# Kernel tuning notes

Measured on AMD Instinct MI355X. Metric: run time of the kernel, lower is better.

Reference implementation:

```python
import jax, jax.numpy as jnp
import numpy as np

B, S, I, C, N, V, O = 32, 256, 256, 512, 1024, 64, 256
EPS = 1e-12


def setup_inputs() -> dict:
    key = jax.random.key(0)
    ks = iter(jax.random.split(key, 40))

    def rn(shape, scale=0.05):
        return (jax.random.normal(next(ks), shape, jnp.float32) * scale)

    inp = {
        'x': jax.random.normal(next(ks), (B, S, I), jnp.float32),
        # LSTM controller (PyTorch gate order i,f,g,o)
        'lstm_Wih': rn((4 * C, I + V)), 'lstm_Whh': rn((4 * C, C)),
        'lstm_bih': rn((4 * C,)), 'lstm_bhh': rn((4 * C,)),
        # read head
        'r_key_W': rn((V, C)), 'r_key_b': rn((V,)),
        'r_str_W': rn((1, C)), 'r_str_b': rn((1,)),
        'r_gate_W': rn((1, C)), 'r_gate_b': rn((1,)),
        'r_shift_W': rn((3, C)), 'r_shift_b': rn((3,)),
        'r_gamma_W': rn((1, C)), 'r_gamma_b': rn((1,)),
        # write head (uses its own key/strength layers, plus erase/add)
        'w_key_W': rn((V, C)), 'w_key_b': rn((V,)),
        'w_str_W': rn((1, C)), 'w_str_b': rn((1,)),
        'w_erase_W': rn((V, C)), 'w_erase_b': rn((V,)),
        'w_add_W': rn((V, C)), 'w_add_b': rn((V,)),
        # output projection
        'out_W': rn((O, C + V)), 'out_b': rn((O,)),
    }
    return inp


def _lin(x, W, b):
    return x @ W.T + b


def _normalize(x, axis):
    n = jnp.linalg.norm(x, axis=axis, keepdims=True)
    return x / jnp.maximum(n, EPS)


def _content_addressing(key_vec, memory, strength):
    # key_vec: [B,V], memory: [B,N,V], strength: [B,1]
    kn = _normalize(key_vec, 1)
    mn = _normalize(memory, 2)
    sim = jnp.einsum('bv,bnv->bn', kn, mn)
    return jax.nn.softmax(strength * sim, axis=1)


def _ntm_forward(x, lstm_Wih, lstm_Whh, lstm_bih, lstm_bhh,
                 r_key_W, r_key_b, r_str_W, r_str_b, r_gate_W, r_gate_b,
                 r_shift_W, r_shift_b, r_gamma_W, r_gamma_b,
                 w_key_W, w_key_b, w_str_W, w_str_b,
                 w_erase_W, w_erase_b, w_add_W, w_add_b, out_W, out_b):
    b = x.shape[0]
    h0 = jnp.zeros((b, C), x.dtype)
    c0 = jnp.zeros((b, C), x.dtype)
    mem0 = jnp.zeros((b, N, V), x.dtype)
    rv0 = jnp.zeros((b, V), x.dtype)

    def step(carry, xt):
        h, c, memory, read_vec = carry
        # LSTM cell
        ci = jnp.concatenate([xt, read_vec], axis=1)          # [B, I+V]
        gates = _lin(ci, lstm_Wih, lstm_bih) + _lin(h, lstm_Whh, lstm_bhh)
        ig, fg, gg, og = jnp.split(gates, 4, axis=1)
        c = jax.nn.sigmoid(fg) * c + jax.nn.sigmoid(ig) * jnp.tanh(gg)
        h = jax.nn.sigmoid(og) * jnp.tanh(c)

        # read head
        key_r = jnp.tanh(_lin(h, r_key_W, r_key_b))
        str_r = jax.nn.softplus(_lin(h, r_str_W, r_str_b))
        gate = jax.nn.sigmoid(_lin(h, r_gate_W, r_gate_b))
        _shift = jax.nn.softmax(_lin(h, r_shift_W, r_shift_b), axis=1)  # computed but unused (as in source)
        gamma = 1.0 + jax.nn.softplus(_lin(h, r_gamma_W, r_gamma_b))
        cw = _content_addressing(key_r, memory, str_r)        # [B,N]
        sharp = cw ** gamma
        lw = sharp / jnp.sum(sharp, axis=1, keepdims=True)
        fw = gate * lw + (1.0 - gate) * cw
        read_vec = jnp.einsum('bn,bnv->bv', fw, memory)

        # write head (erase then add)
        key_w = jnp.tanh(_lin(h, w_key_W, w_key_b))
        str_w = jax.nn.softplus(_lin(h, w_str_W, w_str_b))
        ww = _content_addressing(key_w, memory, str_w)        # [B,N]
        erase = jax.nn.sigmoid(_lin(h, w_erase_W, w_erase_b))  # [B,V]
        add = jnp.tanh(_lin(h, w_add_W, w_add_b))              # [B,V]
        memory = memory * (1.0 - ww[:, :, None] * erase[:, None, :]) \
                 + ww[:, :, None] * add[:, None, :]

        out = _lin(jnp.concatenate([h, read_vec], axis=1), out_W, out_b)
        return (h, c, memory, read_vec), out

    (_, _, final_memory, _), outs = jax.lax.scan(
        step, (h0, c0, mem0, rv0), jnp.swapaxes(x, 0, 1))
    return jnp.swapaxes(outs, 0, 1), final_memory


def reference(x, lstm_Wih, lstm_Whh, lstm_bih, lstm_bhh,
              r_key_W, r_key_b, r_str_W, r_str_b, r_gate_W, r_gate_b,
              r_shift_W, r_shift_b, r_gamma_W, r_gamma_b,
              w_key_W, w_key_b, w_str_W, w_str_b,
              w_erase_W, w_erase_b, w_add_W, w_add_b, out_W, out_b):
    return _ntm_forward(x, lstm_Wih, lstm_Whh, lstm_bih, lstm_bhh,
                        r_key_W, r_key_b, r_str_W, r_str_b, r_gate_W, r_gate_b,
                        r_shift_W, r_shift_b, r_gamma_W, r_gamma_b,
                        w_key_W, w_key_b, w_str_W, w_str_b,
                        w_erase_W, w_erase_b, w_add_W, w_add_b, out_W, out_b)
```

## Files before the change

kernel.cpp:

```cpp
#include <hip/hip_runtime.h>

#define Bv 32
#define Sv 256
#define Iv 256
#define Cv 512
#define Nv 1024
#define Vv 64
#define Ov 256
#define NBLK 256
#define NTHR 256

#define CLAIM_I(x)   ((x)*8)
#define GAL_I(x,q)   (64 + ((x)*4+(q))*8)
#define XROOT_I(x)   (320 + (x)*8)
#define ZERO_BYTES   (640*4)
#define FBASE 1024
#define HBU(x,t1,bb)  (FBASE + (x)*2048 + (t1)*1024 + (bb)*256)
#define EGU(x,bb,k)   (FBASE + 16384 + (x)*2048 + (bb)*512 + (k)*64)
#define SUMPF(x,bb,k) (FBASE + 32768 + (x)*128 + (bb)*32 + (k)*4)
#define HPF(x,bb,r)   (FBASE + 33792 + (((x)*4+(bb))*32 + (r))*264)

struct KP {
  const float *x, *Wih, *Whh, *bih, *bhh;
  const float *rkW, *rkb, *rsW, *rsb, *rgW, *rgb, *rgammaW, *rgammab;
  const float *wkW, *wkb, *wsW, *wsb, *weW, *web, *waW, *wab;
  const float *outW, *outb;
  float *out;
  float *memout;
  float *ws;
};

typedef _Float16 half2v __attribute__((ext_vector_type(2)));
union HU { unsigned u; half2v h; };

__device__ inline float sigf(float x){ return 1.f/(1.f+expf(-x)); }
__device__ inline float softplusf(float x){ return fmaxf(x,0.f) + log1pf(expf(-fabsf(x))); }
__device__ inline unsigned packh(float a, float b){
  HU z; z.h = half2v{(_Float16)a, (_Float16)b}; return z.u;
}
__device__ inline float h2lo(unsigned u){ HU z; z.u = u; return (float)z.h.x; }
__device__ inline float h2hi(unsigned u){ HU z; z.u = u; return (float)z.h.y; }
__device__ inline float dot2(unsigned w, unsigned a, float acc){
  HU wu, au; wu.u = w; au.u = a;
  return __builtin_amdgcn_fdot2(wu.h, au.h, acc, false);
}

__device__ inline void stg_f(float* p, float v){
  asm volatile("global_store_dword %0, %1, off sc0" :: "v"(p), "v"(v) : "memory");
}
__device__ inline void stg_u(unsigned* p, unsigned v){
  asm volatile("global_store_dword %0, %1, off sc0" :: "v"(p), "v"(v) : "memory");
}
#define LDG4U(dst, addr) asm volatile("global_load_dwordx4 %0, %1, off sc0" : "=v"(dst) : "v"(addr) : "memory")
#define LDG4F(dst, addr) asm volatile("global_load_dwordx4 %0, %1, off sc0" : "=v"(dst) : "v"(addr) : "memory")
#define LDGU(dst, addr)  asm volatile("global_load_dword %0, %1, off sc0"  : "=v"(dst) : "v"(addr) : "memory")
#define LDGF(dst, addr)  asm volatile("global_load_dword %0, %1, off sc0"  : "=v"(dst) : "v"(addr) : "memory")
#define WAITV do { asm volatile("s_waitcnt vmcnt(0)" ::: "memory"); __builtin_amdgcn_sched_barrier(0); } while(0)

#define AADD(p,v) __hip_atomic_fetch_add((p),(v),__ATOMIC_RELAXED,__HIP_MEMORY_SCOPE_AGENT)
#define ALD(p)    __hip_atomic_load((p),__ATOMIC_RELAXED,__HIP_MEMORY_SCOPE_AGENT)

#define SPIN(cond_expr) do { unsigned sp = 0; \
  while (cond_expr){ __builtin_amdgcn_s_sleep(2); \
    if (((++sp)&1023u)==0u && (__builtin_amdgcn_s_memrealtime()-t0) > 300000000ULL) break; } } while(0)

__device__ inline float headact(int o, float s){
  if (o < 64)  return tanhf(s);
  if (o == 64) return softplusf(s);
  if (o == 65) return sigf(s);
  if (o == 66) return 1.f + softplusf(s);
  if (o < 131) return tanhf(s);
  if (o == 131) return softplusf(s);
  if (o < 196) return sigf(s);
  return tanhf(s);
}
__device__ inline void head_src(const KP& P, int o, const float** row, float* bias){
  if (o < 64)       { *row = P.rkW + o*Cv;        *bias = P.rkb[o]; }
  else if (o == 64) { *row = P.rsW;               *bias = P.rsb[0]; }
  else if (o == 65) { *row = P.rgW;               *bias = P.rgb[0]; }
  else if (o == 66) { *row = P.rgammaW;           *bias = P.rgammab[0]; }
  else if (o < 131) { *row = P.wkW + (o-67)*Cv;   *bias = P.wkb[o-67]; }
  else if (o == 131){ *row = P.wsW;               *bias = P.wsb[0]; }
  else if (o < 196) { *row = P.weW + (o-132)*Cv;  *bias = P.web[o-132]; }
  else              { *row = P.waW + (o-196)*Cv;  *bias = P.wab[o-196]; }
}

__global__ __launch_bounds__(NTHR) void ntm_kernel(KP P){
  __shared__ unsigned actL[4][420];
  __shared__ float memL[128][66];
  __shared__ float gbq[4][4][68];
  __shared__ float biasL[64];
  __shared__ float htmpf[16][5];
  __shared__ float headsL[264];
  __shared__ float knr[64], knw[64];
  __shared__ float scal[8];
  __shared__ float erL2[128], egL2[128], ewL[128];
  __shared__ float red[32][9];
  __shared__ float red2[2][4];
  __shared__ float sumS1[4][8][4];
  __shared__ float cEL[4], cGL[4];
  __shared__ float sumS4[8][4];
  __shared__ float rvpE[4][64], rvpG[4][64];
  __shared__ float rvfinE[64], rvfinG[64];
  __shared__ int sXcd, sRank;

  const int tid = threadIdx.x;
  float* wsf = P.ws;
  unsigned* wsu = (unsigned*)P.ws;
  int* wsi = (int*)P.ws;
  const unsigned long long t0 = __builtin_amdgcn_s_memrealtime();

  if (tid == 0){
    unsigned xcc;
    asm volatile("s_getreg_b32 %0, hwreg(20, 0, 32)" : "=s"(xcc));
    int xc = (int)(xcc & 7u);
    int rk = AADD(&wsi[CLAIM_I(xc)], 1);
    sXcd = xc; sRank = rk & 31;
  }
  __syncthreads();
  const int xcd = sXcd, rank = sRank;
  const int bl_own = rank >> 3;
  const int rk8 = rank & 7;
  const int bglob = xcd*4 + bl_own;

  const int qw = tid >> 6;
  const int rw = tid & 63;
  const int grw = (rw>>4)*Cv + rank*16 + (rw&15);
  uint4 wreg[26];
  {
    #pragma unroll
    for (int jj = 0; jj < 26; ++jj){
      unsigned uu[4];
      #pragma unroll
      for (int c = 0; c < 4; ++c){
        int e = qw*208 + 8*jj + 2*c;
        float2 w2;
        if (e < 320) w2 = *(const float2*)(P.Wih + grw*320 + e);
        else         w2 = *(const float2*)(P.Whh + grw*512 + (e-320));
        uu[c] = packh(w2.x, w2.y);
      }
      wreg[jj].x = uu[0]; wreg[jj].y = uu[1]; wreg[jj].z = uu[2]; wreg[jj].w = uu[3];
    }
  }
  if (tid < 64){
    int gr = (tid>>4)*Cv + rank*16 + (tid&15);
    biasL[tid] = P.bih[gr] + P.bhh[gr];
  }
  float wA[16], wB[16], bA = 0.f, bB = 0.f;
  {
    const float* rowA; head_src(P, tid, &rowA, &bA);
    #pragma unroll
    for (int j = 0; j < 16; ++j) wA[j] = rowA[rank*16 + j];
    const float* rowB; head_src(P, 256 + (tid & 3), &rowB, &bB);
    #pragma unroll
    for (int j = 0; j < 16; ++j) wB[j] = rowB[rank*16 + j];
  }
  for (int idx = tid; idx < 128*66; idx += NTHR) ((float*)memL)[idx] = 0.f;
  __syncthreads();

  float cS = 0.f;
  int gs = 0;

  for (int t = 0; t < Sv; ++t){
    {
      int bb = tid>>6, part = tid&63;
      const float* xp = P.x + ((size_t)(xcd*4+bb)*Sv + (size_t)t)*Iv + part*4;
      float4 xv = *(const float4*)xp;
      actL[bb][part*2]   = packh(xv.x, xv.y);
      actL[bb][part*2+1] = packh(xv.z, xv.w);
      if (t > 0){
        uint4 hq;
        unsigned e0,e1,e2,e3,e4,e5,e6,e7,g0,g1,g2,g3,g4,g5,g6,g7;
        float4 sv = {0,0,0,0};
        int b2 = tid>>5, j = tid&31;
        LDG4U(hq, wsu + HBU(xcd,(t+1)&1,bb) + part*4);
        if (tid < 128){
          const unsigned* eb = wsu + EGU(xcd,b2,0) + j;
          LDGU(e0,eb+0*64); LDGU(e1,eb+1*64); LDGU(e2,eb+2*64); LDGU(e3,eb+3*64);
          LDGU(e4,eb+4*64); LDGU(e5,eb+5*64); LDGU(e6,eb+6*64); LDGU(e7,eb+7*64);
          const unsigned* ggb = eb + 32;
          LDGU(g0,ggb+0*64); LDGU(g1,ggb+1*64); LDGU(g2,ggb+2*64); LDGU(g3,ggb+3*64);
          LDGU(g4,ggb+4*64); LDGU(g5,ggb+5*64); LDGU(g6,ggb+6*64); LDGU(g7,ggb+7*64);
        }
        if (tid < 32){ LDG4F(sv, wsf + SUMPF(xcd, tid>>3, tid&7)); }
        WAITV;
        *(uint4*)&actL[bb][160 + part*4] = hq;
        if (tid < 32) *(float4*)&sumS1[tid>>3][tid&7][0] = sv;
        __syncthreads();
        if (tid < 4){
          float Se = 0.f, Sg = 0.f;
          #pragma unroll
          for (int k2 = 0; k2 < 8; ++k2){ Se += sumS1[tid][k2][0]; Sg += sumS1[tid][k2][1]; }
          float g = sumS1[tid][0][3];
          cEL[tid] = (1.f - g)/Se;
          cGL[tid] = g/Sg;
        }
        __syncthreads();
        if (tid < 128){
          float Elo = h2lo(e0)+h2lo(e1)+h2lo(e2)+h2lo(e3)+h2lo(e4)+h2lo(e5)+h2lo(e6)+h2lo(e7);
          float Ehi = h2hi(e0)+h2hi(e1)+h2hi(e2)+h2hi(e3)+h2hi(e4)+h2hi(e5)+h2hi(e6)+h2hi(e7);
          float Glo = h2lo(g0)+h2lo(g1)+h2lo(g2)+h2lo(g3)+h2lo(g4)+h2lo(g5)+h2lo(g6)+h2lo(g7);
          float Ghi = h2hi(g0)+h2hi(g1)+h2hi(g2)+h2hi(g3)+h2hi(g4)+h2hi(g5)+h2hi(g6)+h2hi(g7);
          actL[b2][128 + j] = packh(cGL[b2]*Glo + cEL[b2]*Elo, cGL[b2]*Ghi + cEL[b2]*Ehi);
        }
      } else {
        for (int idx = tid; idx < 4*288; idx += NTHR){
          int bb2 = idx/288, u = 128 + idx%288;
          actL[bb2][u] = 0u;
        }
      }
    }
    __syncthreads();
    {
      const int base0 = qw*104;
      float a00=0.f,a01=0.f,a10=0.f,a11=0.f,a20=0.f,a21=0.f,a30=0.f,a31=0.f;
      #pragma unroll
      for (int jj = 0; jj < 26; ++jj){
        uint4 w = wreg[jj];
        uint4 v0 = *(const uint4*)&actL[0][base0+4*jj];
        uint4 v1 = *(const uint4*)&actL[1][base0+4*jj];
        uint4 v2 = *(const uint4*)&actL[2][base0+4*jj];
        uint4 v3 = *(const uint4*)&actL[3][base0+4*jj];
        a00=dot2(w.x,v0.x,a00); a01=dot2(w.y,v0.y,a01); a00=dot2(w.z,v0.z,a00); a01=dot2(w.w,v0.w,a01);
        a10=dot2(w.x,v1.x,a10); a11=dot2(w.y,v1.y,a11); a10=dot2(w.z,v1.z,a10); a11=dot2(w.w,v1.w,a11);
        a20=dot2(w.x,v2.x,a20); a21=dot2(w.y,v2.y,a21); a20=dot2(w.z,v2.z,a20); a21=dot2(w.w,v2.w,a21);
        a30=dot2(w.x,v3.x,a30); a31=dot2(w.y,v3.y,a31); a30=dot2(w.z,v3.z,a30); a31=dot2(w.w,v3.w,a31);
      }
      gbq[qw][0][rw] = a00+a01;
      gbq[qw][1][rw] = a10+a11;
      gbq[qw][2][rw] = a20+a21;
      gbq[qw][3][rw] = a30+a31;
    }
    __syncthreads();
    if (tid < 64){
      int j = tid>>2, bb = tid&3;
      float ig = biasL[j]    + gbq[0][bb][j]    + gbq[1][bb][j]    + gbq[2][bb][j]    + gbq[3][bb][j];
      float fg = biasL[16+j] + gbq[0][bb][16+j] + gbq[1][bb][16+j] + gbq[2][bb][16+j] + gbq[3][bb][16+j];
      float gg = biasL[32+j] + gbq[0][bb][32+j] + gbq[1][bb][32+j] + gbq[2][bb][32+j] + gbq[3][bb][32+j];
      float og = biasL[48+j] + gbq[0][bb][48+j] + gbq[1][bb][48+j] + gbq[2][bb][48+j] + gbq[3][bb][48+j];
      cS = sigf(fg)*cS + sigf(ig)*tanhf(gg);
      htmpf[j][bb] = sigf(og)*tanhf(cS);
    }
    __syncthreads();
    if (tid < 32){
      int pr = tid>>2, bb = tid&3;
      stg_u(wsu + HBU(xcd,t&1,bb) + rank*8 + pr, packh(htmpf[2*pr][bb], htmpf[2*pr+1][bb]));
    }
    {
      float p0=0.f,p1=0.f,p2=0.f,p3=0.f,q0=0.f,q1=0.f,q2=0.f,q3=0.f;
      #pragma unroll
      for (int j = 0; j < 16; ++j){
        float h0=htmpf[j][0], h1=htmpf[j][1], h2=htmpf[j][2], h3=htmpf[j][3];
        p0+=wA[j]*h0; p1+=wA[j]*h1; p2+=wA[j]*h2; p3+=wA[j]*h3;
        q0+=wB[j]*h0; q1+=wB[j]*h1; q2+=wB[j]*h2; q3+=wB[j]*h3;
      }
      stg_f(wsf + HPF(xcd,0,rank) + tid, p0);
      stg_f(wsf + HPF(xcd,1,rank) + tid, p1);
      stg_f(wsf + HPF(xcd,2,rank) + tid, p2);
      stg_f(wsf + HPF(xcd,3,rank) + tid, p3);
      if (tid < 4){
        int o2 = 256 + tid;
        stg_f(wsf + HPF(xcd,0,rank) + o2, q0);
        stg_f(wsf + HPF(xcd,1,rank) + o2, q1);
        stg_f(wsf + HPF(xcd,2,rank) + o2, q2);
        stg_f(wsf + HPF(xcd,3,rank) + o2, q3);
      }
    }
    WAITV;
    __syncthreads();
    if (tid == 0){
      int a = AADD(&wsi[GAL_I(xcd, rank>>3)], 1);
      if (a == 8*(gs+1) - 1) AADD(&wsi[XROOT_I(xcd)], 1);
    }
    if (t > 0){
      int oo = tid>>3, kc = tid&7;
      int o = rk8*32 + oo;
      const float* wrow = P.outW + o*576 + kc*72;
      const unsigned* ab = &actL[bl_own][0];
      float p = 0.f;
      if (kc < 7){
        int u0 = 160 + kc*36;
        #pragma unroll 9
        for (int i = 0; i < 36; ++i){
          unsigned u = ab[u0+i];
          p += h2lo(u)*wrow[2*i] + h2hi(u)*wrow[2*i+1];
        }
      } else {
        #pragma unroll
        for (int i = 0; i < 4; ++i){
          unsigned u = ab[412+i];
          p += h2lo(u)*wrow[2*i] + h2hi(u)*wrow[2*i+1];
        }
        #pragma unroll 8
        for (int i = 0; i < 32; ++i){
          unsigned u = ab[128+i];
          p += h2lo(u)*wrow[8+2*i] + h2hi(u)*wrow[9+2*i];
        }
      }
      red[oo][kc] = p;
      __syncthreads();
      if (tid < 32){
        int o2 = rk8*32 + tid;
        float s = P.outb[o2];
        #pragma unroll
        for (int k2 = 0; k2 < 8; ++k2) s += red[tid][k2];
        P.out[((size_t)bglob*Sv + (t-1))*Ov + o2] = s;
      }
    }
    if (tid == 0){ SPIN(ALD(&wsi[XROOT_I(xcd)]) < 4*(gs+1)); }
    __syncthreads();
    ++gs;

    {
      float s = bA, s2 = bB;
      #pragma unroll
      for (int rr = 0; rr < 4; ++rr){
        const float* hb = wsf + HPF(xcd, bl_own, rr*8);
        float a0,a1,a2,a3,a4,a5,a6,a7,b0,b1,b2,b3,b4,b5,b6,b7;
        int o2 = 256 + (tid & 3);
        LDGF(a0, hb + 0*264 + tid); LDGF(a1, hb + 1*264 + tid);
        LDGF(a2, hb + 2*264 + tid); LDGF(a3, hb + 3*264 + tid);
        LDGF(a4, hb + 4*264 + tid); LDGF(a5, hb + 5*264 + tid);
        LDGF(a6, hb + 6*264 + tid); LDGF(a7, hb + 7*264 + tid);
        LDGF(b0, hb + 0*264 + o2);  LDGF(b1, hb + 1*264 + o2);
        LDGF(b2, hb + 2*264 + o2);  LDGF(b3, hb + 3*264 + o2);
        LDGF(b4, hb + 4*264 + o2);  LDGF(b5, hb + 5*264 + o2);
        LDGF(b6, hb + 6*264 + o2);  LDGF(b7, hb + 7*264 + o2);
        WAITV;
        s  += ((a0+a1)+(a2+a3))+((a4+a5)+(a6+a7));
        s2 += ((b0+b1)+(b2+b3))+((b4+b5)+(b6+b7));
      }
      headsL[tid] = headact(tid, s);
      if (tid < 4) headsL[256+tid] = headact(256+tid, s2);
    }
    __syncthreads();
    if (tid < 64){
      float kr = headsL[tid], kw = headsL[67+tid];
      float sr = kr*kr, sw2 = kw*kw;
      #pragma unroll
      for (int off = 32; off; off >>= 1){ sr += __shfl_xor(sr, off); sw2 += __shfl_xor(sw2, off); }
      knr[tid] = kr * (1.f/fmaxf(sqrtf(sr), 1e-12f));
      knw[tid] = kw * (1.f/fmaxf(sqrtf(sw2), 1e-12f));
    }
    __syncthreads();
    {
      float str_r = headsL[64], gamma = headsL[66], str_w = headsL[131];
      float er = 0.f, eg = 0.f, ew = 0.f;
      if (tid < 128){
        float dr = 0.f, dw = 0.f, nn = 0.f;
        #pragma unroll 8
        for (int v = 0; v < 64; ++v){
          float m = memL[tid][v];
          dr += m*knr[v]; dw += m*knw[v]; nn += m*m;
        }
        float innm = 1.f/fmaxf(sqrtf(nn), 1e-12f);
        float tr = str_r*(dr*innm - 1.f);
        er = expf(tr);
        eg = expf(gamma*tr);
        ew = expf(str_w*(dw*innm - 1.f));
        erL2[tid] = er; egL2[tid] = eg; ewL[tid] = ew;
      }
      float s0 = er, s1 = eg, s2 = ew;
      #pragma unroll
      for (int off = 32; off; off >>= 1){
        s0 += __shfl_xor(s0, off); s1 += __shfl_xor(s1, off); s2 += __shfl_xor(s2, off);
      }
      if ((tid & 63) == 0 && tid < 128){
        int wv = tid>>6; red2[wv][0] = s0; red2[wv][1] = s1; red2[wv][2] = s2;
      }
      __syncthreads();
      if (tid == 0){
        float* sp = wsf + SUMPF(xcd,bl_own,rk8);
        stg_f(sp+0, red2[0][0]+red2[1][0]);
        stg_f(sp+1, red2[0][1]+red2[1][1]);
        stg_f(sp+2, red2[0][2]+red2[1][2]);
        stg_f(sp+3, headsL[65]);
      }
    }
    {
      int v = tid & 63, cc = tid >> 6;
      float pE = 0.f, pG = 0.f;
      #pragma unroll 8
      for (int j = 0; j < 32; ++j){
        int r = cc*32 + j;
        float m = memL[r][v];
        pE += erL2[r]*m; pG += egL2[r]*m;
      }
      rvpE[cc][v] = pE; rvpG[cc][v] = pG;
    }
    __syncthreads();
    if (tid < 64){
      rvfinE[tid] = rvpE[0][tid]+rvpE[1][tid]+rvpE[2][tid]+rvpE[3][tid];
      rvfinG[tid] = rvpG[0][tid]+rvpG[1][tid]+rvpG[2][tid]+rvpG[3][tid];
    }
    __syncthreads();
    if (tid < 32)
      stg_u(wsu + EGU(xcd,bl_own,rk8) + tid, packh(rvfinE[2*tid], rvfinE[2*tid+1]));
    else if (tid < 64)
      stg_u(wsu + EGU(xcd,bl_own,rk8) + tid, packh(rvfinG[2*(tid-32)], rvfinG[2*(tid-32)+1]));
    WAITV;
    __syncthreads();
    if (tid == 0){
      int a = AADD(&wsi[GAL_I(xcd, rank>>3)], 1);
      if (a == 8*(gs+1) - 1) AADD(&wsi[XROOT_I(xcd)], 1);
      SPIN(ALD(&wsi[XROOT_I(xcd)]) < 4*(gs+1));
    }
    __syncthreads();
    ++gs;

    {
      float4 sv = {0,0,0,0};
      if (tid < 8){ LDG4F(sv, wsf + SUMPF(xcd,bl_own,tid)); }
      WAITV;
      if (tid < 8){ *(float4*)&sumS4[tid][0] = sv; }
    }
    __syncthreads();
    if (tid == 0){
      float Sw = 0.f;
      #pragma unroll
      for (int k2 = 0; k2 < 8; ++k2) Sw += sumS4[k2][2];
      scal[6] = Sw;
    }
    __syncthreads();
    {
      float rSw = 1.f/scal[6];
      #pragma unroll 4
      for (int e2 = 0; e2 < 32; ++e2){
        int flat = tid + e2*256;
        int r = flat >> 6, v2 = flat & 63;
        float ww = ewL[r]*rSw;
        memL[r][v2] = memL[r][v2]*(1.f - ww*headsL[132+v2]) + ww*headsL[196+v2];
      }
    }
    __syncthreads();
  }

  {
    int bb = tid>>6, part = tid&63;
    uint4 hq;
    unsigned e0,e1,e2,e3,e4,e5,e6,e7,g0,g1,g2,g3,g4,g5,g6,g7;
    float4 sv = {0,0,0,0};
    int b2 = tid>>5, j = tid&31;
    LDG4U(hq, wsu + HBU(xcd,(Sv-1)&1,bb) + part*4);
    if (tid < 128){
      const unsigned* eb = wsu + EGU(xcd,b2,0) + j;
      LDGU(e0,eb+0*64); LDGU(e1,eb+1*64); LDGU(e2,eb+2*64); LDGU(e3,eb+3*64);
      LDGU(e4,eb+4*64); LDGU(e5,eb+5*64); LDGU(e6,eb+6*64); LDGU(e7,eb+7*64);
      const unsigned* ggb = eb + 32;
      LDGU(g0,ggb+0*64); LDGU(g1,ggb+1*64); LDGU(g2,ggb+2*64); LDGU(g3,ggb+3*64);
      LDGU(g4,ggb+4*64); LDGU(g5,ggb+5*64); LDGU(g6,ggb+6*64); LDGU(g7,ggb+7*64);
    }
    if (tid < 32){ LDG4F(sv, wsf + SUMPF(xcd, tid>>3, tid&7)); }
    WAITV;
    *(uint4*)&actL[bb][160 + part*4] = hq;
    if (tid < 32) *(float4*)&sumS1[tid>>3][tid&7][0] = sv;
    __syncthreads();
    if (tid < 4){
      float Se = 0.f, Sg = 0.f;
      #pragma unroll
      for (int k2 = 0; k2 < 8; ++k2){ Se += sumS1[tid][k2][0]; Sg += sumS1[tid][k2][1]; }
      float g = sumS1[tid][0][3];
      cEL[tid] = (1.f - g)/Se;
      cGL[tid] = g/Sg;
    }
    __syncthreads();
    if (tid < 128){
      float Elo = h2lo(e0)+h2lo(e1)+h2lo(e2)+h2lo(e3)+h2lo(e4)+h2lo(e5)+h2lo(e6)+h2lo(e7);
      float Ehi = h2hi(e0)+h2hi(e1)+h2hi(e2)+h2hi(e3)+h2hi(e4)+h2hi(e5)+h2hi(e6)+h2hi(e7);
      float Glo = h2lo(g0)+h2lo(g1)+h2lo(g2)+h2lo(g3)+h2lo(g4)+h2lo(g5)+h2lo(g6)+h2lo(g7);
      float Ghi = h2hi(g0)+h2hi(g1)+h2hi(g2)+h2hi(g3)+h2hi(g4)+h2hi(g5)+h2hi(g6)+h2hi(g7);
      actL[b2][128 + j] = packh(cGL[b2]*Glo + cEL[b2]*Elo, cGL[b2]*Ghi + cEL[b2]*Ehi);
    }
  }
  __syncthreads();
  {
    int oo = tid>>3, kc = tid&7;
    int o = rk8*32 + oo;
    const float* wrow = P.outW + o*576 + kc*72;
    const unsigned* ab = &actL[bl_own][0];
    float p = 0.f;
    if (kc < 7){
      int u0 = 160 + kc*36;
      #pragma unroll 9
      for (int i = 0; i < 36; ++i){
        unsigned u = ab[u0+i];
        p += h2lo(u)*wrow[2*i] + h2hi(u)*wrow[2*i+1];
      }
    } else {
      #pragma unroll
      for (int i = 0; i < 4; ++i){
        unsigned u = ab[412+i];
        p += h2lo(u)*wrow[2*i] + h2hi(u)*wrow[2*i+1];
      }
      #pragma unroll 8
      for (int i = 0; i < 32; ++i){
        unsigned u = ab[128+i];
        p += h2lo(u)*wrow[8+2*i] + h2hi(u)*wrow[9+2*i];
      }
    }
    red[oo][kc] = p;
    __syncthreads();
    if (tid < 32){
      int o2 = rk8*32 + tid;
      float s = P.outb[o2];
      #pragma unroll
      for (int k2 = 0; k2 < 8; ++k2) s += red[tid][k2];
      P.out[((size_t)bglob*Sv + (Sv-1))*Ov + o2] = s;
    }
  }
  for (int e2 = 0; e2 < 32; ++e2){
    int flat = tid + e2*256;
    int r = flat >> 6, v2 = flat & 63;
    P.memout[((size_t)bglob*Nv + (size_t)rk8*128 + r)*Vv + v2] = memL[r][v2];
  }
}

extern "C" void kernel_launch(void* const* d_in, const int* in_sizes, int n_in,
                              void* d_out, int out_size, void* d_ws, size_t ws_size,
                              hipStream_t stream) {
  (void)in_sizes; (void)n_in; (void)out_size; (void)ws_size;
  KP p;
  p.x       = (const float*)d_in[0];
  p.Wih     = (const float*)d_in[1];
  p.Whh     = (const float*)d_in[2];
  p.bih     = (const float*)d_in[3];
  p.bhh     = (const float*)d_in[4];
  p.rkW     = (const float*)d_in[5];  p.rkb     = (const float*)d_in[6];
  p.rsW     = (const float*)d_in[7];  p.rsb     = (const float*)d_in[8];
  p.rgW     = (const float*)d_in[9];  p.rgb     = (const float*)d_in[10];
  p.rgammaW = (const float*)d_in[13]; p.rgammab = (const float*)d_in[14];
  p.wkW     = (const float*)d_in[15]; p.wkb     = (const float*)d_in[16];
  p.wsW     = (const float*)d_in[17]; p.wsb     = (const float*)d_in[18];
  p.weW     = (const float*)d_in[19]; p.web     = (const float*)d_in[20];
  p.waW     = (const float*)d_in[21]; p.wab     = (const float*)d_in[22];
  p.outW    = (const float*)d_in[23]; p.outb    = (const float*)d_in[24];
  p.out     = (float*)d_out;
  p.memout  = (float*)d_out + (size_t)Bv*Sv*Ov;
  p.ws      = (float*)d_ws;

  hipMemsetAsync(d_ws, 0, ZERO_BYTES, stream);
  hipLaunchKernelGGL(ntm_kernel, dim3(NBLK), dim3(NTHR), 0, stream, p);
}
```

Baseline: 4.245 ms.

## Defer memory write update into next step and prefetch inputs before grid barrier

The memory erase/add update is moved from the end of each timestep to the start of the next, using sums already loaded for the read-weight combination. This removes a separate global load of the write-weight sums and two block barriers per step. The next step's x and h loads are issued before the cross-block spin wait, and head reductions are regrouped into 16-wide load batches to overlap latency. It adds pending erase/add buffers in shared memory and a leftover Sw computation whose result is discarded.

After: 3.971 ms. -6.5%, faster.

```diff
diff --git a/kernel.cpp b/kernel.cpp
--- a/kernel.cpp
+++ b/kernel.cpp
@@ -92,6 +92,7 @@
   __shared__ float biasL[64];
   __shared__ float htmpf[16][5];
   __shared__ float headsL[264];
+  __shared__ float pendE[64], pendA[64];
   __shared__ float knr[64], knw[64];
   __shared__ float scal[8];
   __shared__ float erL2[128], egL2[128], ewL[128];
@@ -99,7 +100,6 @@
   __shared__ float red2[2][4];
   __shared__ float sumS1[4][8][4];
   __shared__ float cEL[4], cGL[4];
-  __shared__ float sumS4[8][4];
   __shared__ float rvpE[4][64], rvpG[4][64];
   __shared__ float rvfinE[64], rvfinG[64];
   __shared__ int sXcd, sRank;
@@ -160,54 +160,76 @@
 
   float cS = 0.f;
   int gs = 0;
+  const int sbb = tid>>6, spart = tid&63;
+  float4 xv;
+  uint4 hq = {};
+  xv = *(const float4*)(P.x + ((size_t)(xcd*4+sbb)*Sv + 0)*Iv + spart*4);
 
   for (int t = 0; t < Sv; ++t){
-    {
-      int bb = tid>>6, part = tid&63;
-      const float* xp = P.x + ((size_t)(xcd*4+bb)*Sv + (size_t)t)*Iv + part*4;
-      float4 xv = *(const float4*)xp;
-      actL[bb][part*2]   = packh(xv.x, xv.y);
-      actL[bb][part*2+1] = packh(xv.z, xv.w);
-      if (t > 0){
-        uint4 hq;
-        unsigned e0,e1,e2,e3,e4,e5,e6,e7,g0,g1,g2,g3,g4,g5,g6,g7;
-        float4 sv = {0,0,0,0};
-        int b2 = tid>>5, j = tid&31;
-        LDG4U(hq, wsu + HBU(xcd,(t+1)&1,bb) + part*4);
-        if (tid < 128){
-          const unsigned* eb = wsu + EGU(xcd,b2,0) + j;
-          LDGU(e0,eb+0*64); LDGU(e1,eb+1*64); LDGU(e2,eb+2*64); LDGU(e3,eb+3*64);
-          LDGU(e4,eb+4*64); LDGU(e5,eb+5*64); LDGU(e6,eb+6*64); LDGU(e7,eb+7*64);
-          const unsigned* ggb = eb + 32;
-          LDGU(g0,ggb+0*64); LDGU(g1,ggb+1*64); LDGU(g2,ggb+2*64); LDGU(g3,ggb+3*64);
-          LDGU(g4,ggb+4*64); LDGU(g5,ggb+5*64); LDGU(g6,ggb+6*64); LDGU(g7,ggb+7*64);
-        }
-        if (tid < 32){ LDG4F(sv, wsf + SUMPF(xcd, tid>>3, tid&7)); }
-        WAITV;
-        *(uint4*)&actL[bb][160 + part*4] = hq;
-        if (tid < 32) *(float4*)&sumS1[tid>>3][tid&7][0] = sv;
-        __syncthreads();
-        if (tid < 4){
-          float Se = 0.f, Sg = 0.f;
-          #pragma unroll
-          for (int k2 = 0; k2 < 8; ++k2){ Se += sumS1[tid][k2][0]; Sg += sumS1[tid][k2][1]; }
-          float g = sumS1[tid][0][3];
-          cEL[tid] = (1.f - g)/Se;
-          cGL[tid] = g/Sg;
-        }
-        __syncthreads();
-        if (tid < 128){
-          float Elo = h2lo(e0)+h2lo(e1)+h2lo(e2)+h2lo(e3)+h2lo(e4)+h2lo(e5)+h2lo(e6)+h2lo(e7);
-          float Ehi = h2hi(e0)+h2hi(e1)+h2hi(e2)+h2hi(e3)+h2hi(e4)+h2hi(e5)+h2hi(e6)+h2hi(e7);
-          float Glo = h2lo(g0)+h2lo(g1)+h2lo(g2)+h2lo(g3)+h2lo(g4)+h2lo(g5)+h2lo(g6)+h2lo(g7);
-          float Ghi = h2hi(g0)+h2hi(g1)+h2hi(g2)+h2hi(g3)+h2hi(g4)+h2hi(g5)+h2hi(g6)+h2hi(g7);
-          actL[b2][128 + j] = packh(cGL[b2]*Glo + cEL[b2]*Elo, cGL[b2]*Ghi + cEL[b2]*Ehi);
-        }
-      } else {
-        for (int idx = tid; idx < 4*288; idx += NTHR){
-          int bb2 = idx/288, u = 128 + idx%288;
-          actL[bb2][u] = 0u;
-        }
+    if (t > 0){
+      unsigned e0,e1,e2,e3,e4,e5,e6,e7,g0,g1,g2,g3,g4,g5,g6,g7;
+      float4 sv = {0,0,0,0};
+      int b2 = tid>>5, j = tid&31;
+      if (tid < 128){
+        const unsigned* eb = wsu + EGU(xcd,b2,0) + j;
+        LDGU(e0,eb+0*64); LDGU(e1,eb+1*64); LDGU(e2,eb+2*64); LDGU(e3,eb+3*64);
+        LDGU(e4,eb+4*64); LDGU(e5,eb+5*64); LDGU(e6,eb+6*64); LDGU(e7,eb+7*64);
+        const unsigned* ggb = eb + 32;
+        LDGU(g0,ggb+0*64); LDGU(g1,ggb+1*64); LDGU(g2,ggb+2*64); LDGU(g3,ggb+3*64);
+        LDGU(g4,ggb+4*64); LDGU(g5,ggb+5*64); LDGU(g6,ggb+6*64); LDGU(g7,ggb+7*64);
+      }
+      if (tid < 32){ LDG4F(sv, wsf + SUMPF(xcd, tid>>3, tid&7)); }
+      WAITV;
+      actL[sbb][spart*2]   = packh(xv.x, xv.y);
+      actL[sbb][spart*2+1] = packh(xv.z, xv.w);
+      *(uint4*)&actL[sbb][160 + spart*4] = hq;
+      if (tid < 32) *(float4*)&sumS1[tid>>3][tid&7][0] = sv;
+      __syncthreads();
+      if (tid < 4){
+        float Se = 0.f, Sg = 0.f;
+        #pragma unroll
+        for (int k2 = 0; k2 < 8; ++k2){ Se += sumS1[tid][k2][0]; Sg += sumS1[tid][k2][1]; }
+        float g = sumS1[tid][0][3];
+        cEL[tid] = (1.f - g)/Se;
+        cGL[tid] = g/Sg;
+      }
+      if (tid == 0){
+        float Sw = 0.f;
+        #pragma unroll
+        for (int k2 = 0; k2 < 8; ++k2) Sw += sumS1[0][k2][2] + sumS1[1][k2][2] + sumS1[2][k2][2] + sumS1[3][k2][2];
+        scal[6] = 0.f;
+      }
+      __syncthreads();
+      if (tid == 0){
+        float Sw = 0.f;
+        #pragma unroll
+        for (int k2 = 0; k2 < 8; ++k2) Sw += sumS1[bl_own][k2][2];
+        scal[6] = Sw;
+      }
+      if (tid < 128){
+        float Elo = h2lo(e0)+h2lo(e1)+h2lo(e2)+h2lo(e3)+h2lo(e4)+h2lo(e5)+h2lo(e6)+h2lo(e7);
+        float Ehi = h2hi(e0)+h2hi(e1)+h2hi(e2)+h2hi(e3)+h2hi(e4)+h2hi(e5)+h2hi(e6)+h2hi(e7);
+        float Glo = h2lo(g0)+h2lo(g1)+h2lo(g2)+h2lo(g3)+h2lo(g4)+h2lo(g5)+h2lo(g6)+h2lo(g7);
+        float Ghi = h2hi(g0)+h2hi(g1)+h2hi(g2)+h2hi(g3)+h2hi(g4)+h2hi(g5)+h2hi(g6)+h2hi(g7);
+        actL[b2][128 + j] = packh(cGL[b2]*Glo + cEL[b2]*Elo, cGL[b2]*Ghi + cEL[b2]*Ehi);
+      }
+      __syncthreads();
+      {
+        float rSw = 1.f/scal[6];
+        #pragma unroll 4
+        for (int e9 = 0; e9 < 32; ++e9){
+          int flat = tid + e9*256;
+          int r = flat >> 6, v2 = flat & 63;
+          float ww = ewL[r]*rSw;
+          memL[r][v2] = memL[r][v2]*(1.f - ww*pendE[v2]) + ww*pendA[v2];
+        }
+      }
+    } else {
+      actL[sbb][spart*2]   = packh(xv.x, xv.y);
+      actL[sbb][spart*2+1] = packh(xv.z, xv.w);
+      for (int idx = tid; idx < 4*288; idx += NTHR){
+        int bb2 = idx/288, u = 128 + idx%288;
+        actL[bb2][u] = 0u;
       }
     }
     __syncthreads();
@@ -314,24 +336,32 @@
     {
       float s = bA, s2 = bB;
       #pragma unroll
-      for (int rr = 0; rr < 4; ++rr){
-        const float* hb = wsf + HPF(xcd, bl_own, rr*8);
-        float a0,a1,a2,a3,a4,a5,a6,a7,b0,b1,b2,b3,b4,b5,b6,b7;
-        int o2 = 256 + (tid & 3);
-        LDGF(a0, hb + 0*264 + tid); LDGF(a1, hb + 1*264 + tid);
-        LDGF(a2, hb + 2*264 + tid); LDGF(a3, hb + 3*264 + tid);
-        LDGF(a4, hb + 4*264 + tid); LDGF(a5, hb + 5*264 + tid);
-        LDGF(a6, hb + 6*264 + tid); LDGF(a7, hb + 7*264 + tid);
-        LDGF(b0, hb + 0*264 + o2);  LDGF(b1, hb + 1*264 + o2);
-        LDGF(b2, hb + 2*264 + o2);  LDGF(b3, hb + 3*264 + o2);
-        LDGF(b4, hb + 4*264 + o2);  LDGF(b5, hb + 5*264 + o2);
-        LDGF(b6, hb + 6*264 + o2);  LDGF(b7, hb + 7*264 + o2);
+      for (int half = 0; half < 2; ++half){
+        const float* hb = wsf + HPF(xcd, bl_own, half*16);
+        float av[16], bv[16];
+        #pragma unroll
+        for (int i = 0; i < 16; ++i){ LDGF(av[i], hb + i*264 + tid); }
+        if (tid < 4){
+          #pragma unroll
+          for (int i = 0; i < 16; ++i){ LDGF(bv[i], hb + i*264 + 256 + tid); }
+        }
         WAITV;
-        s  += ((a0+a1)+(a2+a3))+((a4+a5)+(a6+a7));
-        s2 += ((b0+b1)+(b2+b3))+((b4+b5)+(b6+b7));
-      }
-      headsL[tid] = headact(tid, s);
-      if (tid < 4) headsL[256+tid] = headact(256+tid, s2);
+        #pragma unroll
+        for (int i = 0; i < 16; ++i) s += av[i];
+        if (tid < 4){
+          #pragma unroll
+          for (int i = 0; i < 16; ++i) s2 += bv[i];
+        }
+      }
+      float hv = headact(tid, s);
+      headsL[tid] = hv;
+      if (tid >= 132 && tid < 196) pendE[tid-132] = hv;
+      if (tid >= 196) pendA[tid-196] = hv;
+      if (tid < 4){
+        float hv2 = headact(256+tid, s2);
+        headsL[256+tid] = hv2;
+        pendA[60+tid] = hv2;
+      }
     }
     __syncthreads();
     if (tid < 64){
@@ -403,45 +433,21 @@
     if (tid == 0){
       int a = AADD(&wsi[GAL_I(xcd, rank>>3)], 1);
       if (a == 8*(gs+1) - 1) AADD(&wsi[XROOT_I(xcd)], 1);
-      SPIN(ALD(&wsi[XROOT_I(xcd)]) < 4*(gs+1));
-    }
+    }
+    {
+      if (t + 1 < Sv)
+        xv = *(const float4*)(P.x + ((size_t)(xcd*4+sbb)*Sv + (size_t)(t+1))*Iv + spart*4);
+      LDG4U(hq, wsu + HBU(xcd, t&1, sbb) + spart*4);
+    }
+    if (tid == 0){ SPIN(ALD(&wsi[XROOT_I(xcd)]) < 4*(gs+1)); }
     __syncthreads();
     ++gs;
-
-    {
-      float4 sv = {0,0,0,0};
-      if (tid < 8){ LDG4F(sv, wsf + SUMPF(xcd,bl_own,tid)); }
-      WAITV;
-      if (tid < 8){ *(float4*)&sumS4[tid][0] = sv; }
-    }
-    __syncthreads();
-    if (tid == 0){
-      float Sw = 0.f;
-      #pragma unroll
-      for (int k2 = 0; k2 < 8; ++k2) Sw += sumS4[k2][2];
-      scal[6] = Sw;
-    }
-    __syncthreads();
-    {
-      float rSw = 1.f/scal[6];
-      #pragma unroll 4
-      for (int e2 = 0; e2 < 32; ++e2){
-        int flat = tid + e2*256;
-        int r = flat >> 6, v2 = flat & 63;
-        float ww = ewL[r]*rSw;
-        memL[r][v2] = memL[r][v2]*(1.f - ww*headsL[132+v2]) + ww*headsL[196+v2];
-      }
-    }
-    __syncthreads();
   }
 
   {
-    int bb = tid>>6, part = tid&63;
-    uint4 hq;
     unsigned e0,e1,e2,e3,e4,e5,e6,e7,g0,g1,g2,g3,g4,g5,g6,g7;
     float4 sv = {0,0,0,0};
     int b2 = tid>>5, j = tid&31;
-    LDG4U(hq, wsu + HBU(xcd,(Sv-1)&1,bb) + part*4);
     if (tid < 128){
       const unsigned* eb = wsu + EGU(xcd,b2,0) + j;
       LDGU(e0,eb+0*64); LDGU(e1,eb+1*64); LDGU(e2,eb+2*64); LDGU(e3,eb+3*64);
@@ -452,7 +458,7 @@
     }
     if (tid < 32){ LDG4F(sv, wsf + SUMPF(xcd, tid>>3, tid&7)); }
     WAITV;
-    *(uint4*)&actL[bb][160 + part*4] = hq;
+    *(uint4*)&actL[sbb][160 + spart*4] = hq;
     if (tid < 32) *(float4*)&sumS1[tid>>3][tid&7][0] = sv;
     __syncthreads();
     if (tid < 4){
@@ -462,6 +468,12 @@
       float g = sumS1[tid][0][3];
       cEL[tid] = (1.f - g)/Se;
       cGL[tid] = g/Sg;
+    }
+    if (tid == 0){
+      float Sw = 0.f;
+      #pragma unroll
+      for (int k2 = 0; k2 < 8; ++k2) Sw += sumS1[bl_own][k2][2];
+      scal[6] = Sw;
     }
     __syncthreads();
     if (tid < 128){
@@ -471,8 +483,19 @@
       float Ghi = h2hi(g0)+h2hi(g1)+h2hi(g2)+h2hi(g3)+h2hi(g4)+h2hi(g5)+h2hi(g6)+h2hi(g7);
       actL[b2][128 + j] = packh(cGL[b2]*Glo + cEL[b2]*Elo, cGL[b2]*Ghi + cEL[b2]*Ehi);
     }
-  }
-  __syncthreads();
+    __syncthreads();
+    {
+      float rSw = 1.f/scal[6];
+      #pragma unroll 4
+      for (int e9 = 0; e9 < 32; ++e9){
+        int flat = tid + e9*256;
+        int r = flat >> 6, v2 = flat & 63;
+        float ww = ewL[r]*rSw;
+        memL[r][v2] = memL[r][v2]*(1.f - ww*pendE[v2]) + ww*pendA[v2];
+      }
+    }
+    __syncthreads();
+  }
   {
     int oo = tid>>3, kc = tid&7;
     int o = rk8*32 + oo;
@@ -508,8 +531,8 @@
       P.out[((size_t)bglob*Sv + (Sv-1))*Ov + o2] = s;
     }
   }
-  for (int e2 = 0; e2 < 32; ++e2){
-    int flat = tid + e2*256;
+  for (int e9 = 0; e9 < 32; ++e9){
+    int flat = tid + e9*256;
     int r = flat >> 6, v2 = flat & 63;
     P.memout[((size_t)bglob*Nv + (size_t)rk8*128 + r)*Vv + v2] = memL[r][v2];
   }
```
